# Optimization experiments

Measured on AMD Instinct MI355X. Metric: run time of the kernel, lower is better.

Reference implementation:

```python
import jax, jax.numpy as jnp
import numpy as np

N_SRC0, N_DST0 = 100000, 20000   # block0: 100k src -> 20k dst
N_DST1 = 4096                    # block1: 20k src -> 4096 dst (seed nodes)


def setup_inputs() -> dict:
    key = jax.random.key(0)
    ks = jax.random.split(key, 8)
    E0, E1 = 640000, 131072
    return {
        "features": jax.random.normal(ks[0], (N_SRC0, 256), jnp.float32),
        "W1": jax.random.normal(ks[1], (256, 256), jnp.float32) * (1.0 / np.sqrt(256)),
        "b1": jnp.zeros((256,), jnp.float32),
        "W2": jax.random.normal(ks[2], (256, 128), jnp.float32) * (1.0 / np.sqrt(256)),
        "b2": jnp.zeros((128,), jnp.float32),
        "src0": jax.random.randint(ks[3], (E0,), 0, N_SRC0, jnp.int32),
        "dst0": jax.random.randint(ks[4], (E0,), 0, N_DST0, jnp.int32),
        "src1": jax.random.randint(ks[5], (E1,), 0, N_DST0, jnp.int32),
        "dst1": jax.random.randint(ks[6], (E1,), 0, N_DST1, jnp.int32),
    }


def _graph_conv(src, dst, n_dst, feat, W, b):
    # DGL GraphConv, norm='both': D_out^{-1/2} gather-sum D_in^{-1/2}, then WX+b.
    n_src = feat.shape[0]
    ones = jnp.ones(src.shape[0], feat.dtype)
    out_deg = jax.ops.segment_sum(ones, src, num_segments=n_src)
    norm_src = jnp.clip(out_deg, 1.0, None) ** -0.5          # [n_src]
    h = feat * norm_src[:, None]
    agg = jax.ops.segment_sum(h[src], dst, num_segments=n_dst)  # sparse SpMM
    in_deg = jax.ops.segment_sum(ones, dst, num_segments=n_dst)
    norm_dst = jnp.clip(in_deg, 1.0, None) ** -0.5           # [n_dst]
    return (agg * norm_dst[:, None]) @ W + b


def reference(features, W1, b1, W2, b2, src0, dst0, src1, dst1):
    x = jax.nn.relu(_graph_conv(src0, dst0, N_DST0, features, W1, b1))
    x = _graph_conv(src1, dst1, N_DST1, x, W2, b2)
    return x
```

## Files before the change

### kernel.cpp

```cpp
#include <hip/hip_runtime.h>
#include <hip/hip_bf16.h>

#define K_DIM 256
#define RSTRIDE 128

typedef short bf16x8 __attribute__((ext_vector_type(8)));
typedef float f32x4 __attribute__((ext_vector_type(4)));

static __device__ __forceinline__ unsigned short f2bf(float x) {
    __hip_bfloat16 b = __float2bfloat16(x);
    return *reinterpret_cast<unsigned short*>(&b);
}
static __device__ __forceinline__ float bflo(unsigned int p) {
    return __uint_as_float(p << 16);
}
static __device__ __forceinline__ float bfhi(unsigned int p) {
    return __uint_as_float(p & 0xffff0000u);
}

__global__ void edges_kernel(const int* __restrict__ src0, const int* __restrict__ dst0,
                             int* __restrict__ od0, int* __restrict__ cnt0,
                             int* __restrict__ esrc0, int E0,
                             const int* __restrict__ src1, const int* __restrict__ dst1,
                             int* __restrict__ od1, int* __restrict__ cnt1,
                             int* __restrict__ esrc1, int E1) {
    int i = blockIdx.x * blockDim.x + threadIdx.x;
    if (i < E0) {
        int s = src0[i];
        int d = dst0[i];
        atomicAdd(&od0[s], 1);
        int slot = atomicAdd(&cnt0[d], 1);
        if (slot < RSTRIDE) esrc0[(d << 7) + slot] = s;
    } else if (i < E0 + E1) {
        int e = i - E0;
        int s = src1[e];
        int d = dst1[e];
        atomicAdd(&od1[s], 1);
        int slot = atomicAdd(&cnt1[d], 1);
        if (slot < RSTRIDE) esrc1[(d << 7) + slot] = s;
    }
}

__global__ void castpack_kernel(const float* __restrict__ feat, const int* __restrict__ od0,
                                unsigned short* __restrict__ h, int total, int castBlocks,
                                const float* __restrict__ W1, uint4* __restrict__ pw1,
                                const float* __restrict__ W2, uint4* __restrict__ pw2) {
    if ((int)blockIdx.x < castBlocks) {
        int idx = (blockIdx.x * blockDim.x + threadIdx.x) * 8;
        if (idx >= total) return;
        int row = idx >> 8;
        float ns = rsqrtf((float)max(od0[row], 1));
        const float4 v0 = *reinterpret_cast<const float4*>(feat + idx);
        const float4 v1 = *reinterpret_cast<const float4*>(feat + idx + 4);
        union { ushort4 u4[2]; uint4 u; } o;
        o.u4[0].x = f2bf(v0.x * ns); o.u4[0].y = f2bf(v0.y * ns);
        o.u4[0].z = f2bf(v0.z * ns); o.u4[0].w = f2bf(v0.w * ns);
        o.u4[1].x = f2bf(v1.x * ns); o.u4[1].y = f2bf(v1.y * ns);
        o.u4[1].z = f2bf(v1.z * ns); o.u4[1].w = f2bf(v1.w * ns);
        *reinterpret_cast<uint4*>(h + idx) = o.u;
    } else if ((int)blockIdx.x < castBlocks + 32) {
        int idx = ((int)blockIdx.x - castBlocks) * blockDim.x + threadIdx.x;
        int lane = idx & 63;
        int kt = (idx >> 6) & 7;
        int nt = idx >> 9;
        int n = nt * 16 + (lane & 15);
        int k = kt * 32 + (lane >> 4) * 8;
        union { unsigned short us[8]; uint4 u; } o;
#pragma unroll
        for (int j = 0; j < 8; ++j) o.us[j] = f2bf(W1[(size_t)(k + j) * 256 + n]);
        pw1[idx] = o.u;
    } else {
        int idx = ((int)blockIdx.x - castBlocks - 32) * blockDim.x + threadIdx.x;
        int lane = idx & 63;
        int kt = (idx >> 6) & 7;
        int nt = idx >> 9;
        int n = nt * 16 + (lane & 15);
        int k = kt * 32 + (lane >> 4) * 8;
        union { unsigned short us[8]; uint4 u; } o;
#pragma unroll
        for (int j = 0; j < 8; ++j) o.us[j] = f2bf(W2[(size_t)(k + j) * 128 + n]);
        pw2[idx] = o.u;
    }
}

__global__ __launch_bounds__(256) void gather_bf16_kernel(
        const unsigned short* __restrict__ hfeat, const int* __restrict__ esrc,
        const int* __restrict__ cnt, unsigned short* __restrict__ aggb, int n_dst) {
    int row = blockIdx.x * (blockDim.x >> 6) + (threadIdx.x >> 6);
    int lane = threadIdx.x & 63;
    if (row >= n_dst) return;
    const int c = cnt[row];
    const int cend = min(c, RSTRIDE);
    const int* __restrict__ ep = esrc + ((size_t)row << 7);
    float a0 = 0.f, a1 = 0.f, a2 = 0.f, a3 = 0.f;
    int i = 0;
    for (; i + 3 < cend; i += 4) {
        int s0 = ep[i];
        int s1 = ep[i + 1];
        int s2 = ep[i + 2];
        int s3 = ep[i + 3];
        const uint2 p0 = *reinterpret_cast<const uint2*>(hfeat + (((size_t)s0) << 8) + lane * 4);
        const uint2 p1 = *reinterpret_cast<const uint2*>(hfeat + (((size_t)s1) << 8) + lane * 4);
        const uint2 p2 = *reinterpret_cast<const uint2*>(hfeat + (((size_t)s2) << 8) + lane * 4);
        const uint2 p3 = *reinterpret_cast<const uint2*>(hfeat + (((size_t)s3) << 8) + lane * 4);
        a0 += (bflo(p0.x) + bflo(p1.x)) + (bflo(p2.x) + bflo(p3.x));
        a1 += (bfhi(p0.x) + bfhi(p1.x)) + (bfhi(p2.x) + bfhi(p3.x));
        a2 += (bflo(p0.y) + bflo(p1.y)) + (bflo(p2.y) + bflo(p3.y));
        a3 += (bfhi(p0.y) + bfhi(p1.y)) + (bfhi(p2.y) + bfhi(p3.y));
    }
    for (; i < cend; ++i) {
        int s0 = ep[i];
        const uint2 p0 = *reinterpret_cast<const uint2*>(hfeat + (((size_t)s0) << 8) + lane * 4);
        a0 += bflo(p0.x);
        a1 += bfhi(p0.x);
        a2 += bflo(p0.y);
        a3 += bfhi(p0.y);
    }
    float nd = rsqrtf((float)max(c, 1));
    ushort4 o;
    o.x = f2bf(a0 * nd);
    o.y = f2bf(a1 * nd);
    o.z = f2bf(a2 * nd);
    o.w = f2bf(a3 * nd);
    *reinterpret_cast<ushort4*>(aggb + (((size_t)row) << 8) + lane * 4) = o;
}

__global__ __launch_bounds__(256) void gemm0_mfma_kernel(
        const unsigned short* __restrict__ hA, const uint4* __restrict__ pW,
        const float* __restrict__ bias, const int* __restrict__ od1,
        unsigned short* __restrict__ out, int M) {
    const int m0 = blockIdx.x * 16;
    const int w = threadIdx.x >> 6;
    const int lane = threadIdx.x & 63;

    bf16x8 a[8];
    const unsigned short* ap = hA + (size_t)(m0 + (lane & 15)) * K_DIM + (lane >> 4) * 8;
#pragma unroll
    for (int kt = 0; kt < 8; ++kt)
        a[kt] = *reinterpret_cast<const bf16x8*>(ap + kt * 32);

    const int rbase = m0 + (lane >> 4) * 4;
    float nsv[4];
#pragma unroll
    for (int r = 0; r < 4; ++r) nsv[r] = rsqrtf((float)max(od1[rbase + r], 1));

#pragma unroll
    for (int nt = 0; nt < 4; ++nt) {
        const int n0 = w * 64 + nt * 16;
        f32x4 acc = {0.f, 0.f, 0.f, 0.f};
#pragma unroll
        for (int kt = 0; kt < 8; ++kt) {
            bf16x8 b = *reinterpret_cast<const bf16x8*>(&pW[((size_t)(n0 >> 4) * 8 + kt) * 64 + lane]);
            acc = __builtin_amdgcn_mfma_f32_16x16x32_bf16(a[kt], b, acc, 0, 0, 0);
        }
        const int col = n0 + (lane & 15);
        const float bv = bias[col];
#pragma unroll
        for (int r = 0; r < 4; ++r) {
            float v = fmaxf(acc[r] + bv, 0.0f) * nsv[r];
            out[(size_t)(rbase + r) * K_DIM + col] = f2bf(v);
        }
    }
}

__global__ __launch_bounds__(256) void gemm1_mfma_kernel(
        const unsigned short* __restrict__ hA, const uint4* __restrict__ pW,
        const float* __restrict__ bias, float* __restrict__ out, int M) {
    const int m0 = blockIdx.x * 16;
    const int w = threadIdx.x >> 6;
    const int lane = threadIdx.x & 63;

    bf16x8 a[8];
    const unsigned short* ap = hA + (size_t)(m0 + (lane & 15)) * K_DIM + (lane >> 4) * 8;
#pragma unroll
    for (int kt = 0; kt < 8; ++kt)
        a[kt] = *reinterpret_cast<const bf16x8*>(ap + kt * 32);

    const int rbase = m0 + (lane >> 4) * 4;
#pragma unroll
    for (int nt = 0; nt < 2; ++nt) {
        const int n0 = w * 32 + nt * 16;
        f32x4 acc = {0.f, 0.f, 0.f, 0.f};
#pragma unroll
        for (int kt = 0; kt < 8; ++kt) {
            bf16x8 b = *reinterpret_cast<const bf16x8*>(&pW[((size_t)(n0 >> 4) * 8 + kt) * 64 + lane]);
            acc = __builtin_amdgcn_mfma_f32_16x16x32_bf16(a[kt], b, acc, 0, 0, 0);
        }
        const int col = n0 + (lane & 15);
        const float bv = bias[col];
#pragma unroll
        for (int r = 0; r < 4; ++r)
            out[(size_t)(rbase + r) * 128 + col] = acc[r] + bv;
    }
}

__global__ __launch_bounds__(256) void gatherf_kernel(
        const float* __restrict__ feat, const int* __restrict__ esrc,
        const int* __restrict__ cnt, const int* __restrict__ od,
        float* __restrict__ outbuf, int n_dst) {
    int row = blockIdx.x * (blockDim.x >> 6) + (threadIdx.x >> 6);
    int lane = threadIdx.x & 63;
    if (row >= n_dst) return;
    const int c = cnt[row];
    const int cend = min(c, RSTRIDE);
    const int* __restrict__ ep = esrc + ((size_t)row << 7);
    float4 acc = {0.f, 0.f, 0.f, 0.f};
    for (int i = 0; i < cend; ++i) {
        int s0 = ep[i];
        float n0 = rsqrtf((float)max(od[s0], 1));
        const float4 v0 = *reinterpret_cast<const float4*>(feat + (((size_t)s0) << 8) + lane * 4);
        acc.x = fmaf(v0.x, n0, acc.x); acc.y = fmaf(v0.y, n0, acc.y);
        acc.z = fmaf(v0.z, n0, acc.z); acc.w = fmaf(v0.w, n0, acc.w);
    }
    float nd = rsqrtf((float)max(c, 1));
    float4 o = {acc.x * nd, acc.y * nd, acc.z * nd, acc.w * nd};
    *reinterpret_cast<float4*>(outbuf + (((size_t)row) << 8) + lane * 4) = o;
}

template <int ROWS, int NCOLS, bool RELU>
__global__ __launch_bounds__(NCOLS) void gemm_kernel(
        const float* __restrict__ A, const float* __restrict__ W,
        const float* __restrict__ bias, float* __restrict__ out, int M) {
    const int row0 = blockIdx.x * ROWS;
    const int c = threadIdx.x;
    const float* __restrict__ Ablk = A + (size_t)row0 * K_DIM;
    const float* __restrict__ Wc = W + c;

    float acc[ROWS];
#pragma unroll
    for (int r = 0; r < ROWS; ++r) acc[r] = 0.0f;

    float w0 = Wc[0];
    float w1 = Wc[NCOLS];
    float w2 = Wc[2 * NCOLS];
    float w3 = Wc[3 * NCOLS];

#pragma unroll 2
    for (int k = 0; k < K_DIM - 4; k += 4) {
        const float* p = Wc + (size_t)(k + 4) * NCOLS;
        float n0 = p[0];
        float n1 = p[NCOLS];
        float n2 = p[2 * NCOLS];
        float n3 = p[3 * NCOLS];
#pragma unroll
        for (int r = 0; r < ROWS; ++r) {
            const float4 a = *reinterpret_cast<const float4*>(Ablk + r * K_DIM + k);
            acc[r] = fmaf(a.x, w0, acc[r]);
            acc[r] = fmaf(a.y, w1, acc[r]);
            acc[r] = fmaf(a.z, w2, acc[r]);
            acc[r] = fmaf(a.w, w3, acc[r]);
        }
        w0 = n0; w1 = n1; w2 = n2; w3 = n3;
    }
    {
        const int k = K_DIM - 4;
#pragma unroll
        for (int r = 0; r < ROWS; ++r) {
            const float4 a = *reinterpret_cast<const float4*>(Ablk + r * K_DIM + k);
            acc[r] = fmaf(a.x, w0, acc[r]);
            acc[r] = fmaf(a.y, w1, acc[r]);
            acc[r] = fmaf(a.z, w2, acc[r]);
            acc[r] = fmaf(a.w, w3, acc[r]);
        }
    }

    const float b = bias[c];
#pragma unroll
    for (int r = 0; r < ROWS; ++r) {
        float v = acc[r] + b;
        if (RELU) v = fmaxf(v, 0.0f);
        out[(size_t)(row0 + r) * NCOLS + c] = v;
    }
}

extern "C" void kernel_launch(void* const* d_in, const int* in_sizes, int n_in,
                              void* d_out, int out_size, void* d_ws, size_t ws_size,
                              hipStream_t stream) {
    const float* features = (const float*)d_in[0];
    const float* W1 = (const float*)d_in[1];
    const float* b1 = (const float*)d_in[2];
    const float* W2 = (const float*)d_in[3];
    const float* b2 = (const float*)d_in[4];
    const int* src0 = (const int*)d_in[5];
    const int* dst0 = (const int*)d_in[6];
    const int* src1 = (const int*)d_in[7];
    const int* dst1 = (const int*)d_in[8];
    const int E0 = in_sizes[5];
    const int E1 = in_sizes[7];
    const int NSRC0 = 100000, NDST0 = 20000, NDST1 = 4096;

    char* ws = (char*)d_ws;
    size_t off = 0;
    auto carve = [&](size_t bytes) -> void* {
        void* p = ws + off;
        off = (off + bytes + 255) & ~(size_t)255;
        return p;
    };
    int* od0  = (int*)carve((size_t)NSRC0 * 4);
    int* od1  = (int*)carve((size_t)NDST0 * 4);
    int* cnt0 = (int*)carve((size_t)NDST0 * 4);
    int* cnt1 = (int*)carve((size_t)NDST1 * 4);
    const size_t zero_span = off;
    uint4* pW1  = (uint4*)carve((size_t)8192 * 16);
    uint4* pW2  = (uint4*)carve((size_t)4096 * 16);
    int* esrc0p = (int*)carve((size_t)NDST0 * RSTRIDE * 4);
    int* esrc1p = (int*)carve((size_t)NDST1 * RSTRIDE * 4);
    unsigned short* aggb = (unsigned short*)carve((size_t)NDST0 * K_DIM * 2);
    const size_t hfeat_bytes = (size_t)NSRC0 * K_DIM * 2;
    const size_t xbufb_bytes = (size_t)NDST0 * K_DIM * 2;
    const size_t agg1b_bytes = (size_t)NDST1 * K_DIM * 2;
    const size_t need_bf16 = off + (hfeat_bytes > xbufb_bytes + agg1b_bytes
                                        ? hfeat_bytes : xbufb_bytes + agg1b_bytes);
    (void)n_in; (void)out_size;

    hipMemsetAsync(ws, 0, zero_span, stream);

    edges_kernel<<<(E0 + E1 + 255) / 256, 256, 0, stream>>>(
        src0, dst0, od0, cnt0, esrc0p, E0,
        src1, dst1, od1, cnt1, esrc1p, E1);

    if (ws_size >= need_bf16) {
        unsigned short* hfeat = (unsigned short*)(ws + off);
        unsigned short* xbufb = (unsigned short*)(ws + off);
        unsigned short* agg1b = (unsigned short*)(ws + off + xbufb_bytes);

        const int total_f = NSRC0 * K_DIM;
        const int castBlocks = (total_f / 8 + 255) / 256;
        castpack_kernel<<<castBlocks + 48, 256, 0, stream>>>(features, od0, hfeat, total_f,
                                                             castBlocks, W1, pW1, W2, pW2);
        gather_bf16_kernel<<<(NDST0 + 3) / 4, 256, 0, stream>>>(hfeat, esrc0p, cnt0,
                                                                aggb, NDST0);
        gemm0_mfma_kernel<<<NDST0 / 16, 256, 0, stream>>>(aggb, pW1, b1, od1, xbufb, NDST0);
        gather_bf16_kernel<<<(NDST1 + 3) / 4, 256, 0, stream>>>(xbufb, esrc1p, cnt1,
                                                                agg1b, NDST1);
        gemm1_mfma_kernel<<<NDST1 / 16, 256, 0, stream>>>(agg1b, pW2, b2,
                                                          (float*)d_out, NDST1);
    } else {
        float* agg0 = (float*)carve((size_t)NDST0 * K_DIM * 4);
        float* xbuf = (float*)carve((size_t)NDST0 * K_DIM * 4);
        float* agg1 = (float*)carve((size_t)NDST1 * K_DIM * 4);
        gatherf_kernel<<<(NDST0 + 3) / 4, 256, 0, stream>>>(features, esrc0p, cnt0, od0,
                                                            agg0, NDST0);
        gemm_kernel<16, 256, true><<<NDST0 / 16, 256, 0, stream>>>(agg0, W1, b1, xbuf, NDST0);
        gatherf_kernel<<<(NDST1 + 3) / 4, 256, 0, stream>>>(xbuf, esrc1p, cnt1, od1,
                                                            agg1, NDST1);
        gemm_kernel<4, 128, false><<<NDST1 / 4, 128, 0, stream>>>(agg1, W2, b2,
                                                                  (float*)d_out, NDST1);
    }
}
```

Measured before the change: 331.1 us.

## Fuse edge counting with feature cast and move source normalization into gather

The edge-scatter pass and the bf16 cast/weight-pack pass now run as independent block ranges of one kernel. This is possible because the source out-degree scaling is no longer applied during the cast. Instead, the first-layer gather reads od0 per edge and applies rsqrt as an FMA weight. This removes one kernel launch and the serialization between edge counting and the 100k-row cast, so both can overlap. The cost is an extra scattered od0 load and rsqrt per gathered edge.

```diff
diff --git a/kernel.cpp b/kernel.cpp
--- a/kernel.cpp
+++ b/kernel.cpp
@@ -16,6 +16,226 @@
 }
 static __device__ __forceinline__ float bfhi(unsigned int p) {
     return __uint_as_float(p & 0xffff0000u);
+}
+
+__global__ void mega_kernel(
+        const int* __restrict__ src0, const int* __restrict__ dst0,
+        int* __restrict__ od0, int* __restrict__ cnt0, int* __restrict__ esrc0, int E0,
+        const int* __restrict__ src1, const int* __restrict__ dst1,
+        int* __restrict__ od1, int* __restrict__ cnt1, int* __restrict__ esrc1, int E1,
+        int edgeBlocks,
+        const float* __restrict__ feat, unsigned short* __restrict__ h, int total_f,
+        int castBlocks,
+        const float* __restrict__ W1, uint4* __restrict__ pw1,
+        const float* __restrict__ W2, uint4* __restrict__ pw2) {
+    const int b = blockIdx.x;
+    if (b < edgeBlocks) {
+        int i = b * blockDim.x + threadIdx.x;
+        if (i < E0) {
+            int s = src0[i];
+            int d = dst0[i];
+            atomicAdd(&od0[s], 1);
+            int slot = atomicAdd(&cnt0[d], 1);
+            if (slot < RSTRIDE) esrc0[(d << 7) + slot] = s;
+        } else if (i < E0 + E1) {
+            int e = i - E0;
+            int s = src1[e];
+            int d = dst1[e];
+            atomicAdd(&od1[s], 1);
+            int slot = atomicAdd(&cnt1[d], 1);
+            if (slot < RSTRIDE) esrc1[(d << 7) + slot] = s;
+        }
+    } else if (b < edgeBlocks + castBlocks) {
+        int idx = ((b - edgeBlocks) * blockDim.x + threadIdx.x) * 8;
+        if (idx >= total_f) return;
+        const float4 v0 = *reinterpret_cast<const float4*>(feat + idx);
+        const float4 v1 = *reinterpret_cast<const float4*>(feat + idx + 4);
+        union { ushort4 u4[2]; uint4 u; } o;
+        o.u4[0].x = f2bf(v0.x); o.u4[0].y = f2bf(v0.y);
+        o.u4[0].z = f2bf(v0.z); o.u4[0].w = f2bf(v0.w);
+        o.u4[1].x = f2bf(v1.x); o.u4[1].y = f2bf(v1.y);
+        o.u4[1].z = f2bf(v1.z); o.u4[1].w = f2bf(v1.w);
+        *reinterpret_cast<uint4*>(h + idx) = o.u;
+    } else if (b < edgeBlocks + castBlocks + 32) {
+        int idx = (b - edgeBlocks - castBlocks) * blockDim.x + threadIdx.x;
+        int lane = idx & 63;
+        int kt = (idx >> 6) & 7;
+        int nt = idx >> 9;
+        int n = nt * 16 + (lane & 15);
+        int k = kt * 32 + (lane >> 4) * 8;
+        union { unsigned short us[8]; uint4 u; } o;
+#pragma unroll
+        for (int j = 0; j < 8; ++j) o.us[j] = f2bf(W1[(size_t)(k + j) * 256 + n]);
+        pw1[idx] = o.u;
+    } else {
+        int idx = (b - edgeBlocks - castBlocks - 32) * blockDim.x + threadIdx.x;
+        int lane = idx & 63;
+        int kt = (idx >> 6) & 7;
+        int nt = idx >> 9;
+        int n = nt * 16 + (lane & 15);
+        int k = kt * 32 + (lane >> 4) * 8;
+        union { unsigned short us[8]; uint4 u; } o;
+#pragma unroll
+        for (int j = 0; j < 8; ++j) o.us[j] = f2bf(W2[(size_t)(k + j) * 128 + n]);
+        pw2[idx] = o.u;
+    }
+}
+
+template <bool NORM>
+__global__ __launch_bounds__(256) void gather_bf16_kernel(
+        const unsigned short* __restrict__ hfeat, const int* __restrict__ esrc,
+        const int* __restrict__ cnt, const int* __restrict__ od,
+        unsigned short* __restrict__ aggb, int n_dst) {
+    int row = blockIdx.x * (blockDim.x >> 6) + (threadIdx.x >> 6);
+    int lane = threadIdx.x & 63;
+    if (row >= n_dst) return;
+    const int c = cnt[row];
+    const int cend = min(c, RSTRIDE);
+    const int* __restrict__ ep = esrc + ((size_t)row << 7);
+    float a0 = 0.f, a1 = 0.f, a2 = 0.f, a3 = 0.f;
+    int i = 0;
+    for (; i + 3 < cend; i += 4) {
+        int s0 = ep[i];
+        int s1 = ep[i + 1];
+        int s2 = ep[i + 2];
+        int s3 = ep[i + 3];
+        float n0 = NORM ? rsqrtf((float)max(od[s0], 1)) : 1.0f;
+        float n1 = NORM ? rsqrtf((float)max(od[s1], 1)) : 1.0f;
+        float n2 = NORM ? rsqrtf((float)max(od[s2], 1)) : 1.0f;
+        float n3 = NORM ? rsqrtf((float)max(od[s3], 1)) : 1.0f;
+        const uint2 p0 = *reinterpret_cast<const uint2*>(hfeat + (((size_t)s0) << 8) + lane * 4);
+        const uint2 p1 = *reinterpret_cast<const uint2*>(hfeat + (((size_t)s1) << 8) + lane * 4);
+        const uint2 p2 = *reinterpret_cast<const uint2*>(hfeat + (((size_t)s2) << 8) + lane * 4);
+        const uint2 p3 = *reinterpret_cast<const uint2*>(hfeat + (((size_t)s3) << 8) + lane * 4);
+        if (NORM) {
+            a0 = fmaf(bflo(p0.x), n0, a0); a1 = fmaf(bfhi(p0.x), n0, a1);
+            a2 = fmaf(bflo(p0.y), n0, a2); a3 = fmaf(bfhi(p0.y), n0, a3);
+            a0 = fmaf(bflo(p1.x), n1, a0); a1 = fmaf(bfhi(p1.x), n1, a1);
+            a2 = fmaf(bflo(p1.y), n1, a2); a3 = fmaf(bfhi(p1.y), n1, a3);
+            a0 = fmaf(bflo(p2.x), n2, a0); a1 = fmaf(bfhi(p2.x), n2, a1);
+            a2 = fmaf(bflo(p2.y), n2, a2); a3 = fmaf(bfhi(p2.y), n2, a3);
+            a0 = fmaf(bflo(p3.x), n3, a0); a1 = fmaf(bfhi(p3.x), n3, a1);
+            a2 = fmaf(bflo(p3.y), n3, a2); a3 = fmaf(bfhi(p3.y), n3, a3);
+        } else {
+            a0 += (bflo(p0.x) + bflo(p1.x)) + (bflo(p2.x) + bflo(p3.x));
+            a1 += (bfhi(p0.x) + bfhi(p1.x)) + (bfhi(p2.x) + bfhi(p3.x));
+            a2 += (bflo(p0.y) + bflo(p1.y)) + (bflo(p2.y) + bflo(p3.y));
+            a3 += (bfhi(p0.y) + bfhi(p1.y)) + (bfhi(p2.y) + bfhi(p3.y));
+        }
+    }
+    for (; i < cend; ++i) {
+        int s0 = ep[i];
+        float n0 = NORM ? rsqrtf((float)max(od[s0], 1)) : 1.0f;
+        const uint2 p0 = *reinterpret_cast<const uint2*>(hfeat + (((size_t)s0) << 8) + lane * 4);
+        if (NORM) {
+            a0 = fmaf(bflo(p0.x), n0, a0); a1 = fmaf(bfhi(p0.x), n0, a1);
+            a2 = fmaf(bflo(p0.y), n0, a2); a3 = fmaf(bfhi(p0.y), n0, a3);
+        } else {
+            a0 += bflo(p0.x);
+            a1 += bfhi(p0.x);
+            a2 += bflo(p0.y);
+            a3 += bfhi(p0.y);
+        }
+    }
+    float nd = rsqrtf((float)max(c, 1));
+    ushort4 o;
+    o.x = f2bf(a0 * nd);
+    o.y = f2bf(a1 * nd);
+    o.z = f2bf(a2 * nd);
+    o.w = f2bf(a3 * nd);
+    *reinterpret_cast<ushort4*>(aggb + (((size_t)row) << 8) + lane * 4) = o;
+}
+
+__global__ __launch_bounds__(256) void gemm0_mfma_kernel(
+        const unsigned short* __restrict__ hA, const uint4* __restrict__ pW,
+        const float* __restrict__ bias, const int* __restrict__ od1,
+        unsigned short* __restrict__ out, int M) {
+    const int m0 = blockIdx.x * 16;
+    const int w = threadIdx.x >> 6;
+    const int lane = threadIdx.x & 63;
+
+    bf16x8 a[8];
+    const unsigned short* ap = hA + (size_t)(m0 + (lane & 15)) * K_DIM + (lane >> 4) * 8;
+#pragma unroll
+    for (int kt = 0; kt < 8; ++kt)
+        a[kt] = *reinterpret_cast<const bf16x8*>(ap + kt * 32);
+
+    const int rbase = m0 + (lane >> 4) * 4;
+    float nsv[4];
+#pragma unroll
+    for (int r = 0; r < 4; ++r) nsv[r] = rsqrtf((float)max(od1[rbase + r], 1));
+
+#pragma unroll
+    for (int nt = 0; nt < 4; ++nt) {
+        const int n0 = w * 64 + nt * 16;
+        f32x4 acc = {0.f, 0.f, 0.f, 0.f};
+#pragma unroll
+        for (int kt = 0; kt < 8; ++kt) {
+            bf16x8 b = *reinterpret_cast<const bf16x8*>(&pW[((size_t)(n0 >> 4) * 8 + kt) * 64 + lane]);
+            acc = __builtin_amdgcn_mfma_f32_16x16x32_bf16(a[kt], b, acc, 0, 0, 0);
+        }
+        const int col = n0 + (lane & 15);
+        const float bv = bias[col];
+#pragma unroll
+        for (int r = 0; r < 4; ++r) {
+            float v = fmaxf(acc[r] + bv, 0.0f) * nsv[r];
+            out[(size_t)(rbase + r) * K_DIM + col] = f2bf(v);
+        }
+    }
+}
+
+__global__ __launch_bounds__(256) void gemm1_mfma_kernel(
+        const unsigned short* __restrict__ hA, const uint4* __restrict__ pW,
+        const float* __restrict__ bias, float* __restrict__ out, int M) {
+    const int m0 = blockIdx.x * 16;
+    const int w = threadIdx.x >> 6;
+    const int lane = threadIdx.x & 63;
+
+    bf16x8 a[8];
+    const unsigned short* ap = hA + (size_t)(m0 + (lane & 15)) * K_DIM + (lane >> 4) * 8;
+#pragma unroll
+    for (int kt = 0; kt < 8; ++kt)
+        a[kt] = *reinterpret_cast<const bf16x8*>(ap + kt * 32);
+
+    const int rbase = m0 + (lane >> 4) * 4;
+#pragma unroll
+    for (int nt = 0; nt < 2; ++nt) {
+        const int n0 = w * 32 + nt * 16;
+        f32x4 acc = {0.f, 0.f, 0.f, 0.f};
+#pragma unroll
+        for (int kt = 0; kt < 8; ++kt) {
+            bf16x8 b = *reinterpret_cast<const bf16x8*>(&pW[((size_t)(n0 >> 4) * 8 + kt) * 64 + lane]);
+            acc = __builtin_amdgcn_mfma_f32_16x16x32_bf16(a[kt], b, acc, 0, 0, 0);
+        }
+        const int col = n0 + (lane & 15);
+        const float bv = bias[col];
+#pragma unroll
+        for (int r = 0; r < 4; ++r)
+            out[(size_t)(rbase + r) * 128 + col] = acc[r] + bv;
+    }
+}
+
+__global__ __launch_bounds__(256) void gatherf_kernel(
+        const float* __restrict__ feat, const int* __restrict__ esrc,
+        const int* __restrict__ cnt, const int* __restrict__ od,
+        float* __restrict__ outbuf, int n_dst) {
+    int row = blockIdx.x * (blockDim.x >> 6) + (threadIdx.x >> 6);
+    int lane = threadIdx.x & 63;
+    if (row >= n_dst) return;
+    const int c = cnt[row];
+    const int cend = min(c, RSTRIDE);
+    const int* __restrict__ ep = esrc + ((size_t)row << 7);
+    float4 acc = {0.f, 0.f, 0.f, 0.f};
+    for (int i = 0; i < cend; ++i) {
+        int s0 = ep[i];
+        float n0 = rsqrtf((float)max(od[s0], 1));
+        const float4 v0 = *reinterpret_cast<const float4*>(feat + (((size_t)s0) << 8) + lane * 4);
+        acc.x = fmaf(v0.x, n0, acc.x); acc.y = fmaf(v0.y, n0, acc.y);
+        acc.z = fmaf(v0.z, n0, acc.z); acc.w = fmaf(v0.w, n0, acc.w);
+    }
+    float nd = rsqrtf((float)max(c, 1));
+    float4 o = {acc.x * nd, acc.y * nd, acc.z * nd, acc.w * nd};
+    *reinterpret_cast<float4*>(outbuf + (((size_t)row) << 8) + lane * 4) = o;
 }
 
 __global__ void edges_kernel(const int* __restrict__ src0, const int* __restrict__ dst0,
@@ -39,182 +259,6 @@
         int slot = atomicAdd(&cnt1[d], 1);
         if (slot < RSTRIDE) esrc1[(d << 7) + slot] = s;
     }
-}
-
-__global__ void castpack_kernel(const float* __restrict__ feat, const int* __restrict__ od0,
-                                unsigned short* __restrict__ h, int total, int castBlocks,
-                                const float* __restrict__ W1, uint4* __restrict__ pw1,
-                                const float* __restrict__ W2, uint4* __restrict__ pw2) {
-    if ((int)blockIdx.x < castBlocks) {
-        int idx = (blockIdx.x * blockDim.x + threadIdx.x) * 8;
-        if (idx >= total) return;
-        int row = idx >> 8;
-        float ns = rsqrtf((float)max(od0[row], 1));
-        const float4 v0 = *reinterpret_cast<const float4*>(feat + idx);
-        const float4 v1 = *reinterpret_cast<const float4*>(feat + idx + 4);
-        union { ushort4 u4[2]; uint4 u; } o;
-        o.u4[0].x = f2bf(v0.x * ns); o.u4[0].y = f2bf(v0.y * ns);
-        o.u4[0].z = f2bf(v0.z * ns); o.u4[0].w = f2bf(v0.w * ns);
-        o.u4[1].x = f2bf(v1.x * ns); o.u4[1].y = f2bf(v1.y * ns);
-        o.u4[1].z = f2bf(v1.z * ns); o.u4[1].w = f2bf(v1.w * ns);
-        *reinterpret_cast<uint4*>(h + idx) = o.u;
-    } else if ((int)blockIdx.x < castBlocks + 32) {
-        int idx = ((int)blockIdx.x - castBlocks) * blockDim.x + threadIdx.x;
-        int lane = idx & 63;
-        int kt = (idx >> 6) & 7;
-        int nt = idx >> 9;
-        int n = nt * 16 + (lane & 15);
-        int k = kt * 32 + (lane >> 4) * 8;
-        union { unsigned short us[8]; uint4 u; } o;
-#pragma unroll
-        for (int j = 0; j < 8; ++j) o.us[j] = f2bf(W1[(size_t)(k + j) * 256 + n]);
-        pw1[idx] = o.u;
-    } else {
-        int idx = ((int)blockIdx.x - castBlocks - 32) * blockDim.x + threadIdx.x;
-        int lane = idx & 63;
-        int kt = (idx >> 6) & 7;
-        int nt = idx >> 9;
-        int n = nt * 16 + (lane & 15);
-        int k = kt * 32 + (lane >> 4) * 8;
-        union { unsigned short us[8]; uint4 u; } o;
-#pragma unroll
-        for (int j = 0; j < 8; ++j) o.us[j] = f2bf(W2[(size_t)(k + j) * 128 + n]);
-        pw2[idx] = o.u;
-    }
-}
-
-__global__ __launch_bounds__(256) void gather_bf16_kernel(
-        const unsigned short* __restrict__ hfeat, const int* __restrict__ esrc,
-        const int* __restrict__ cnt, unsigned short* __restrict__ aggb, int n_dst) {
-    int row = blockIdx.x * (blockDim.x >> 6) + (threadIdx.x >> 6);
-    int lane = threadIdx.x & 63;
-    if (row >= n_dst) return;
-    const int c = cnt[row];
-    const int cend = min(c, RSTRIDE);
-    const int* __restrict__ ep = esrc + ((size_t)row << 7);
-    float a0 = 0.f, a1 = 0.f, a2 = 0.f, a3 = 0.f;
-    int i = 0;
-    for (; i + 3 < cend; i += 4) {
-        int s0 = ep[i];
-        int s1 = ep[i + 1];
-        int s2 = ep[i + 2];
-        int s3 = ep[i + 3];
-        const uint2 p0 = *reinterpret_cast<const uint2*>(hfeat + (((size_t)s0) << 8) + lane * 4);
-        const uint2 p1 = *reinterpret_cast<const uint2*>(hfeat + (((size_t)s1) << 8) + lane * 4);
-        const uint2 p2 = *reinterpret_cast<const uint2*>(hfeat + (((size_t)s2) << 8) + lane * 4);
-        const uint2 p3 = *reinterpret_cast<const uint2*>(hfeat + (((size_t)s3) << 8) + lane * 4);
-        a0 += (bflo(p0.x) + bflo(p1.x)) + (bflo(p2.x) + bflo(p3.x));
-        a1 += (bfhi(p0.x) + bfhi(p1.x)) + (bfhi(p2.x) + bfhi(p3.x));
-        a2 += (bflo(p0.y) + bflo(p1.y)) + (bflo(p2.y) + bflo(p3.y));
-        a3 += (bfhi(p0.y) + bfhi(p1.y)) + (bfhi(p2.y) + bfhi(p3.y));
-    }
-    for (; i < cend; ++i) {
-        int s0 = ep[i];
-        const uint2 p0 = *reinterpret_cast<const uint2*>(hfeat + (((size_t)s0) << 8) + lane * 4);
-        a0 += bflo(p0.x);
-        a1 += bfhi(p0.x);
-        a2 += bflo(p0.y);
-        a3 += bfhi(p0.y);
-    }
-    float nd = rsqrtf((float)max(c, 1));
-    ushort4 o;
-    o.x = f2bf(a0 * nd);
-    o.y = f2bf(a1 * nd);
-    o.z = f2bf(a2 * nd);
-    o.w = f2bf(a3 * nd);
-    *reinterpret_cast<ushort4*>(aggb + (((size_t)row) << 8) + lane * 4) = o;
-}
-
-__global__ __launch_bounds__(256) void gemm0_mfma_kernel(
-        const unsigned short* __restrict__ hA, const uint4* __restrict__ pW,
-        const float* __restrict__ bias, const int* __restrict__ od1,
-        unsigned short* __restrict__ out, int M) {
-    const int m0 = blockIdx.x * 16;
-    const int w = threadIdx.x >> 6;
-    const int lane = threadIdx.x & 63;
-
-    bf16x8 a[8];
-    const unsigned short* ap = hA + (size_t)(m0 + (lane & 15)) * K_DIM + (lane >> 4) * 8;
-#pragma unroll
-    for (int kt = 0; kt < 8; ++kt)
-        a[kt] = *reinterpret_cast<const bf16x8*>(ap + kt * 32);
-
-    const int rbase = m0 + (lane >> 4) * 4;
-    float nsv[4];
-#pragma unroll
-    for (int r = 0; r < 4; ++r) nsv[r] = rsqrtf((float)max(od1[rbase + r], 1));
-
-#pragma unroll
-    for (int nt = 0; nt < 4; ++nt) {
-        const int n0 = w * 64 + nt * 16;
-        f32x4 acc = {0.f, 0.f, 0.f, 0.f};
-#pragma unroll
-        for (int kt = 0; kt < 8; ++kt) {
-            bf16x8 b = *reinterpret_cast<const bf16x8*>(&pW[((size_t)(n0 >> 4) * 8 + kt) * 64 + lane]);
-            acc = __builtin_amdgcn_mfma_f32_16x16x32_bf16(a[kt], b, acc, 0, 0, 0);
-        }
-        const int col = n0 + (lane & 15);
-        const float bv = bias[col];
-#pragma unroll
-        for (int r = 0; r < 4; ++r) {
-            float v = fmaxf(acc[r] + bv, 0.0f) * nsv[r];
-            out[(size_t)(rbase + r) * K_DIM + col] = f2bf(v);
-        }
-    }
-}
-
-__global__ __launch_bounds__(256) void gemm1_mfma_kernel(
-        const unsigned short* __restrict__ hA, const uint4* __restrict__ pW,
-        const float* __restrict__ bias, float* __restrict__ out, int M) {
-    const int m0 = blockIdx.x * 16;
-    const int w = threadIdx.x >> 6;
-    const int lane = threadIdx.x & 63;
-
-    bf16x8 a[8];
-    const unsigned short* ap = hA + (size_t)(m0 + (lane & 15)) * K_DIM + (lane >> 4) * 8;
-#pragma unroll
-    for (int kt = 0; kt < 8; ++kt)
-        a[kt] = *reinterpret_cast<const bf16x8*>(ap + kt * 32);
-
-    const int rbase = m0 + (lane >> 4) * 4;
-#pragma unroll
-    for (int nt = 0; nt < 2; ++nt) {
-        const int n0 = w * 32 + nt * 16;
-        f32x4 acc = {0.f, 0.f, 0.f, 0.f};
-#pragma unroll
-        for (int kt = 0; kt < 8; ++kt) {
-            bf16x8 b = *reinterpret_cast<const bf16x8*>(&pW[((size_t)(n0 >> 4) * 8 + kt) * 64 + lane]);
-            acc = __builtin_amdgcn_mfma_f32_16x16x32_bf16(a[kt], b, acc, 0, 0, 0);
-        }
-        const int col = n0 + (lane & 15);
-        const float bv = bias[col];
-#pragma unroll
-        for (int r = 0; r < 4; ++r)
-            out[(size_t)(rbase + r) * 128 + col] = acc[r] + bv;
-    }
-}
-
-__global__ __launch_bounds__(256) void gatherf_kernel(
-        const float* __restrict__ feat, const int* __restrict__ esrc,
-        const int* __restrict__ cnt, const int* __restrict__ od,
-        float* __restrict__ outbuf, int n_dst) {
-    int row = blockIdx.x * (blockDim.x >> 6) + (threadIdx.x >> 6);
-    int lane = threadIdx.x & 63;
-    if (row >= n_dst) return;
-    const int c = cnt[row];
-    const int cend = min(c, RSTRIDE);
-    const int* __restrict__ ep = esrc + ((size_t)row << 7);
-    float4 acc = {0.f, 0.f, 0.f, 0.f};
-    for (int i = 0; i < cend; ++i) {
-        int s0 = ep[i];
-        float n0 = rsqrtf((float)max(od[s0], 1));
-        const float4 v0 = *reinterpret_cast<const float4*>(feat + (((size_t)s0) << 8) + lane * 4);
-        acc.x = fmaf(v0.x, n0, acc.x); acc.y = fmaf(v0.y, n0, acc.y);
-        acc.z = fmaf(v0.z, n0, acc.z); acc.w = fmaf(v0.w, n0, acc.w);
-    }
-    float nd = rsqrtf((float)max(c, 1));
-    float4 o = {acc.x * nd, acc.y * nd, acc.z * nd, acc.w * nd};
-    *reinterpret_cast<float4*>(outbuf + (((size_t)row) << 8) + lane * 4) = o;
 }
 
 template <int ROWS, int NCOLS, bool RELU>
@@ -315,30 +359,33 @@
 
     hipMemsetAsync(ws, 0, zero_span, stream);
 
-    edges_kernel<<<(E0 + E1 + 255) / 256, 256, 0, stream>>>(
-        src0, dst0, od0, cnt0, esrc0p, E0,
-        src1, dst1, od1, cnt1, esrc1p, E1);
-
     if (ws_size >= need_bf16) {
         unsigned short* hfeat = (unsigned short*)(ws + off);
         unsigned short* xbufb = (unsigned short*)(ws + off);
         unsigned short* agg1b = (unsigned short*)(ws + off + xbufb_bytes);
 
         const int total_f = NSRC0 * K_DIM;
+        const int edgeBlocks = (E0 + E1 + 255) / 256;
         const int castBlocks = (total_f / 8 + 255) / 256;
-        castpack_kernel<<<castBlocks + 48, 256, 0, stream>>>(features, od0, hfeat, total_f,
-                                                             castBlocks, W1, pW1, W2, pW2);
-        gather_bf16_kernel<<<(NDST0 + 3) / 4, 256, 0, stream>>>(hfeat, esrc0p, cnt0,
-                                                                aggb, NDST0);
+        mega_kernel<<<edgeBlocks + castBlocks + 48, 256, 0, stream>>>(
+            src0, dst0, od0, cnt0, esrc0p, E0,
+            src1, dst1, od1, cnt1, esrc1p, E1, edgeBlocks,
+            features, hfeat, total_f, castBlocks,
+            W1, pW1, W2, pW2);
+        gather_bf16_kernel<true><<<(NDST0 + 3) / 4, 256, 0, stream>>>(
+            hfeat, esrc0p, cnt0, od0, aggb, NDST0);
         gemm0_mfma_kernel<<<NDST0 / 16, 256, 0, stream>>>(aggb, pW1, b1, od1, xbufb, NDST0);
-        gather_bf16_kernel<<<(NDST1 + 3) / 4, 256, 0, stream>>>(xbufb, esrc1p, cnt1,
-                                                                agg1b, NDST1);
+        gather_bf16_kernel<false><<<(NDST1 + 3) / 4, 256, 0, stream>>>(
+            xbufb, esrc1p, cnt1, nullptr, agg1b, NDST1);
         gemm1_mfma_kernel<<<NDST1 / 16, 256, 0, stream>>>(agg1b, pW2, b2,
                                                           (float*)d_out, NDST1);
     } else {
         float* agg0 = (float*)carve((size_t)NDST0 * K_DIM * 4);
         float* xbuf = (float*)carve((size_t)NDST0 * K_DIM * 4);
         float* agg1 = (float*)carve((size_t)NDST1 * K_DIM * 4);
+        edges_kernel<<<(E0 + E1 + 255) / 256, 256, 0, stream>>>(
+            src0, dst0, od0, cnt0, esrc0p, E0,
+            src1, dst1, od1, cnt1, esrc1p, E1);
         gatherf_kernel<<<(NDST0 + 3) / 4, 256, 0, stream>>>(features, esrc0p, cnt0, od0,
                                                             agg0, NDST0);
         gemm_kernel<16, 256, true><<<NDST0 / 16, 256, 0, stream>>>(agg0, W1, b1, xbuf, NDST0);
```

Measured after the change: 314.8 us. 1.05x faster.
